# Optimization experiments

Hardware: AMD Instinct MI355X
Metric: run time of the kernel (lower is better)

## Reference

```python
import jax, jax.numpy as jnp
import numpy as np

HIDDEN = 1024
NUM_HEADS = 16
HEAD_DIM = HIDDEN // NUM_HEADS  # 64
B, S = 2, 2048


def setup_inputs() -> dict:
    key = jax.random.key(0)
    ks = jax.random.split(key, 10)
    sd = 1.0 / np.sqrt(HIDDEN)
    x = jax.random.normal(ks[0], (B, S, HIDDEN), dtype=jnp.float32)
    # per-head projections stacked over head axis: [H, hidden, head_dim]
    Wq = jax.random.normal(ks[1], (NUM_HEADS, HIDDEN, HEAD_DIM), dtype=jnp.float32) * sd
    Wk = jax.random.normal(ks[2], (NUM_HEADS, HIDDEN, HEAD_DIM), dtype=jnp.float32) * sd
    Wv = jax.random.normal(ks[3], (NUM_HEADS, HIDDEN, HEAD_DIM), dtype=jnp.float32) * sd
    bq = jax.random.normal(ks[4], (NUM_HEADS, HEAD_DIM), dtype=jnp.float32) * sd
    bk = jax.random.normal(ks[5], (NUM_HEADS, HEAD_DIM), dtype=jnp.float32) * sd
    bv = jax.random.normal(ks[6], (NUM_HEADS, HEAD_DIM), dtype=jnp.float32) * sd
    # output projection: [all_head_size, hidden]
    Wo = jax.random.normal(ks[7], (HIDDEN, HIDDEN), dtype=jnp.float32) * sd
    bo = jax.random.normal(ks[8], (HIDDEN,), dtype=jnp.float32) * sd
    return {"x": x, "Wq": Wq, "bq": bq, "Wk": Wk, "bk": bk,
            "Wv": Wv, "bv": bv, "Wo": Wo, "bo": bo}


def reference(x, Wq, bq, Wk, bk, Wv, bv, Wo, bo):
    # Fused-across-heads equivalent of the per-head Python loop.
    # q,k,v: [B, H, S, Dh]
    q = jnp.einsum('bsd,hde->bhse', x, Wq) + bq[None, :, None, :]
    k = jnp.einsum('bsd,hde->bhse', x, Wk) + bk[None, :, None, :]
    v = jnp.einsum('bsd,hde->bhse', x, Wv) + bv[None, :, None, :]
    scale = 1.0 / jnp.sqrt(jnp.asarray(HEAD_DIM, dtype=x.dtype))
    scores = jnp.einsum('bhse,bhte->bhst', q, k) * scale  # [B,H,S,S]
    probs = jax.nn.softmax(scores, axis=-1)               # dropout=0 (eval)
    ctx = jnp.einsum('bhst,bhte->bhse', probs, v)         # [B,H,S,Dh]
    # concat heads on last dim (head order matches torch.cat over heads)
    ctx = jnp.transpose(ctx, (0, 2, 1, 3)).reshape(x.shape[0], x.shape[1], -1)
    out = ctx @ Wo + bo                                   # output projection
    return out
```

## Files before the change

kernel.cpp:

```cpp
#include <hip/hip_runtime.h>
#include <cstdint>

typedef unsigned short u16;
typedef __attribute__((ext_vector_type(8))) short short8;
typedef __attribute__((ext_vector_type(4))) short short4v;
typedef __attribute__((ext_vector_type(4))) float f32x4;
typedef __attribute__((ext_vector_type(4))) unsigned short u16x4;

__device__ __forceinline__ u16 f2bf(float x) {
    unsigned int u = __float_as_uint(x);
    u += 0x7fffu + ((u >> 16) & 1u);
    return (u16)(u >> 16);
}

__device__ __forceinline__ float fexp2(float x) {
#if __has_builtin(__builtin_amdgcn_exp2f)
    return __builtin_amdgcn_exp2f(x);
#else
    return exp2f(x);
#endif
}

__device__ __forceinline__ unsigned pack_bf16(float a, float b) {
    unsigned ua = __float_as_uint(a) + 0x8000u;
    unsigned ub = __float_as_uint(b) + 0x8000u;
    return __builtin_amdgcn_perm(ub, ua, 0x07060302u);
}

#if __has_builtin(__builtin_amdgcn_mfma_f32_16x16x16bf16_1k)
__device__ __forceinline__ f32x4 mfma16(short4v a, short4v b, f32x4 c) {
    return __builtin_amdgcn_mfma_f32_16x16x16bf16_1k(a, b, c, 0, 0, 0);
}
#else
__device__ __forceinline__ f32x4 mfma16(short4v a, short4v b, f32x4 c) {
    short8 a8 = {a[0], a[1], a[2], a[3], 0, 0, 0, 0};
    short8 b8 = {b[0], b[1], b[2], b[3], 0, 0, 0, 0};
    return __builtin_amdgcn_mfma_f32_16x16x32_bf16(a8, b8, c, 0, 0, 0);
}
#endif

__device__ __forceinline__ void gload_lds16(const u16* g, u16* l) {
    __builtin_amdgcn_global_load_lds(
        (const __attribute__((address_space(1))) void*)(g),
        (__attribute__((address_space(3))) void*)(l),
        16, 0, 0);
}

__global__ __launch_bounds__(256) void prep_kernel(
    const float* __restrict__ x,
    const float* __restrict__ Wq, const float* __restrict__ Wk,
    const float* __restrict__ Wv, const float* __restrict__ Wo,
    u16* __restrict__ xb, u16* __restrict__ wqkv, u16* __restrict__ wot)
{
    __shared__ u16 tile[64][65];
    const int z = blockIdx.z;
    const int tc = threadIdx.x & 63, tr = threadIdx.x >> 6;

    if (z == 1) {
        const int blk = blockIdx.y * 16 + blockIdx.x;
        const int base = (blk * 256 + threadIdx.x) * 4;
        #pragma unroll
        for (int i = 0; i < 16; ++i) {
            const int idx = base + i * 262144;
            float4 v = *(const float4*)(x + idx);
            u16x4 o;
            o.x = f2bf(v.x); o.y = f2bf(v.y); o.z = f2bf(v.z); o.w = f2bf(v.w);
            *(u16x4*)(xb + idx) = o;
        }
        return;
    }

    const float* src;
    u16* dst;
    int C, R, rb, cb;
    if (z == 0) {
        src = Wo; dst = wot; C = 1024; R = 1024;
        rb = blockIdx.x * 64; cb = blockIdx.y * 64;
    } else {
        const float* W = (z == 2) ? Wq : (z == 3) ? Wk : Wv;
        const int head = blockIdx.y;
        src = W + head * 65536;
        dst = wqkv + (size_t)(z - 2) * 1048576 + head * 65536;
        C = 64; R = 1024;
        rb = blockIdx.x * 64; cb = 0;
    }
    #pragma unroll
    for (int i = 0; i < 64; i += 4)
        tile[tr + i][tc] = f2bf(src[(size_t)(rb + tr + i) * C + (cb + tc)]);
    __syncthreads();
    #pragma unroll
    for (int i = 0; i < 64; i += 4)
        dst[(size_t)(cb + tr + i) * R + (rb + tc)] = tile[tc][tr + i];
}

__global__ __launch_bounds__(512, 2) void gemm_qkv_kernel(
    const u16* __restrict__ X, const u16* __restrict__ W,
    const float* __restrict__ bq, const float* __restrict__ bk,
    const float* __restrict__ bv,
    u16* __restrict__ qo, u16* __restrict__ ko, u16* __restrict__ vto)
{
    __shared__ __align__(16) u16 lds[32768];
    const int tid = threadIdx.x;
    const int lane = tid & 63;
    const int wid = tid >> 6;
    const int wm = wid >> 2;
    const int wn = wid & 3;
    const int c = lane & 15, qd = lane >> 4;

    const int id = (blockIdx.x & 7) * 24 + (blockIdx.x >> 3);
    const int m0 = (id / 12) * 256;
    const int n0 = (id % 12) * 256;

    const u16* Xb = X + (size_t)m0 * 1024;
    const u16* Wb = W + (size_t)n0 * 1024;

    const int srow = tid >> 2;
    const int scg  = (lane & 3) ^ ((lane >> 3) & 3);
    const int cof = (qd ^ ((c >> 1) & 3)) * 8;
    const int rA0 = wm * 128 + c;
    const int rB0 = wn * 64 + c;

    auto stage = [&](int t, int p) {
        const int pb = p * 16384;
        #pragma unroll
        for (int j = 0; j < 2; ++j) {
            const int row = j * 128 + srow;
            const u16* gs = Xb + (size_t)row * 1024 + t * 32 + scg * 8;
            gload_lds16(gs, &lds[pb + (j * 512 + tid) * 8]);
            const u16* gw = Wb + (size_t)row * 1024 + t * 32 + scg * 8;
            gload_lds16(gw, &lds[pb + 8192 + (j * 512 + tid) * 8]);
        }
    };

    f32x4 acc[8][4];
    #pragma unroll
    for (int mi = 0; mi < 8; ++mi)
        #pragma unroll
        for (int ni = 0; ni < 4; ++ni) acc[mi][ni] = f32x4{0.f, 0.f, 0.f, 0.f};

    auto body = [&](int t) {
        const int pb = (t & 1) * 16384;
        __builtin_amdgcn_sched_barrier(0);
        __builtin_amdgcn_s_barrier();
        __builtin_amdgcn_sched_barrier(0);
        short8 af[8], bf[4];
        #pragma unroll
        for (int mi = 0; mi < 8; ++mi)
            af[mi] = *(const short8*)&lds[pb + (rA0 + mi * 16) * 32 + cof];
        #pragma unroll
        for (int ni = 0; ni < 4; ++ni)
            bf[ni] = *(const short8*)&lds[pb + 8192 + (rB0 + ni * 16) * 32 + cof];
        __builtin_amdgcn_s_setprio(1);
        #pragma unroll
        for (int mi = 0; mi < 8; ++mi)
            #pragma unroll
            for (int ni = 0; ni < 4; ++ni)
                acc[mi][ni] = __builtin_amdgcn_mfma_f32_16x16x32_bf16(af[mi], bf[ni], acc[mi][ni], 0, 0, 0);
        __builtin_amdgcn_s_setprio(0);
        __builtin_amdgcn_sched_barrier(0);
        __builtin_amdgcn_s_barrier();
    };

    stage(0, 0);
    stage(1, 1);
    __builtin_amdgcn_sched_barrier(0);

    for (int t = 0; t < 31; ++t) {
        __builtin_amdgcn_s_waitcnt(0xF74);
        body(t);
        if (t < 30) stage(t + 2, t & 1);
        __builtin_amdgcn_sched_barrier(0);
    }
    __builtin_amdgcn_s_waitcnt(0xF70);
    body(31);

    #pragma unroll
    for (int mi = 0; mi < 8; ++mi) {
        const int mbase = m0 + wm * 128 + mi * 16 + qd * 4;
        const int b = mbase >> 11;
        #pragma unroll
        for (int ni = 0; ni < 4; ++ni) {
            const int n = n0 + wn * 64 + ni * 16 + c;
            const int mat = n >> 10;
            const int idx = n & 1023;
            const int h = idx >> 6, e = idx & 63;
            const float bias = (mat == 0 ? bq : (mat == 1 ? bk : bv))[idx];
            if (mat == 2) {
                const int s = mbase & 2047;
                u16x4 pv;
                pv.x = f2bf(acc[mi][ni][0] + bias);
                pv.y = f2bf(acc[mi][ni][1] + bias);
                pv.z = f2bf(acc[mi][ni][2] + bias);
                pv.w = f2bf(acc[mi][ni][3] + bias);
                *(u16x4*)(vto + ((((size_t)(b * 16 + h) * 128 + (s >> 4)) * 64 + e) * 16
                                 + (s & 15))) = pv;
            } else {
                const float scale = (mat == 0) ? 0.18033688011112042f : 1.0f;
                u16* dst = (mat == 0) ? qo : ko;
                #pragma unroll
                for (int r = 0; r < 4; ++r) {
                    const int s = (mbase + r) & 2047;
                    dst[((size_t)((b * 16 + h) * 2048 + s)) * 64 + e] =
                        f2bf((acc[mi][ni][r] + bias) * scale);
                }
            }
        }
    }
}

__global__ __launch_bounds__(256, 3) void flash_kernel(
    const u16* __restrict__ Q,
    const u16* __restrict__ K,
    const u16* __restrict__ V2,
    u16* __restrict__ ctx)
{
    __shared__ __align__(16) char pool[34816];
    u16* stage = (u16*)pool;
    float (*Os)[64][66] = (float (*)[64][66])pool;
    float (*Ls)[64] = (float (*)[64])(pool + 33792);

    const int tid = threadIdx.x, lane = tid & 63, w = tid >> 6;
    const int c = lane & 15, qd = lane >> 4;
    const int bid = blockIdx.x;
    const int r5 = bid & 31;
    const int bh = (r5 & 7) * 4 + (r5 >> 3);
    const int q0 = (bid >> 5) * 64;
    const int b = bh >> 4, h = bh & 15;
    const u16* Qh = Q + (size_t)bh * 2048 * 64;
    const u16* Kh = K + (size_t)bh * 2048 * 64;
    const u16* Vh = V2 + (size_t)bh * 128 * 1024;

    u16* Kst = stage + w * 3072;

    const int krow8 = lane >> 3;
    const int kgc = (lane & 7) ^ (krow8 & 7);
    const int voff = c * 16 + qd * 4;

    short8 qf[4][2];
    #pragma unroll
    for (int qb = 0; qb < 4; ++qb)
        #pragma unroll
        for (int kb = 0; kb < 2; ++kb)
            qf[qb][kb] = *(const short8*)&Qh[(size_t)(q0 + qb * 16 + c) * 64 + kb * 32 + qd * 8];

    f32x4 o[4][4];
    float lsum[4];
    #pragma unroll
    for (int mt = 0; mt < 4; ++mt)
        #pragma unroll
        for (int qb = 0; qb < 4; ++qb) o[mt][qb] = f32x4{0.f, 0.f, 0.f, 0.f};
    #pragma unroll
    for (int qb = 0; qb < 4; ++qb) lsum[qb] = 0.f;

    #pragma unroll
    for (int j = 0; j < 2; ++j) {
        const int row = j * 8 + krow8;
        gload_lds16(Kh + (size_t)(w * 512 + row) * 64 + kgc * 8,
                    Kst + j * 512 + lane * 8);
    }
    short4v vA[4], vB[4];
    {
        const u16* vb = Vh + (size_t)(w * 32) * 1024 + voff;
        #pragma unroll
        for (int mt = 0; mt < 4; ++mt)
            vA[mt] = *(const short4v*)(vb + mt * 256);
    }
    #pragma unroll
    for (int j = 0; j < 2; ++j) {
        const int row = j * 8 + krow8;
        gload_lds16(Kh + (size_t)(w * 512 + 16 + row) * 64 + kgc * 8,
                    Kst + 1024 + j * 512 + lane * 8);
    }

    int cur = 0;
    auto body = [&](int it, short4v (&VC)[4], short4v (&VN)[4]) {
        u16* Kb = Kst + cur * 1024;

        __builtin_amdgcn_s_waitcnt(0xF74);
        __builtin_amdgcn_sched_barrier(0);

        short8 kf[2];
        #pragma unroll
        for (int kb = 0; kb < 2; ++kb)
            kf[kb] = *(const short8*)&Kb[c * 64 + ((4 * kb + qd) ^ (c & 7)) * 8];

        __builtin_amdgcn_sched_barrier(0);

        {
            const int itn = (it + 1) & 31;
            const u16* vb = Vh + (size_t)(w * 32 + itn) * 1024 + voff;
            #pragma unroll
            for (int mt = 0; mt < 4; ++mt)
                VN[mt] = *(const short4v*)(vb + mt * 256);
        }
        {
            const int itn = (it + 2) & 31;
            const int t0n = w * 512 + itn * 16;
            const int nslot = (cur >= 1) ? cur - 1 : 2;
            u16* Kn = Kst + nslot * 1024;
            #pragma unroll
            for (int j = 0; j < 2; ++j) {
                const int row = j * 8 + krow8;
                gload_lds16(Kh + (size_t)(t0n + row) * 64 + kgc * 8,
                            Kn + j * 512 + lane * 8);
            }
        }

        f32x4 sc[4];
        #pragma unroll
        for (int qb = 0; qb < 4; ++qb) {
            sc[qb] = f32x4{0.f, 0.f, 0.f, 0.f};
            sc[qb] = __builtin_amdgcn_mfma_f32_16x16x32_bf16(kf[0], qf[qb][0], sc[qb], 0, 0, 0);
            sc[qb] = __builtin_amdgcn_mfma_f32_16x16x32_bf16(kf[1], qf[qb][1], sc[qb], 0, 0, 0);
        }

        short4v pb[4];
        #pragma unroll
        for (int qb = 0; qb < 4; ++qb) {
            float p0 = fexp2(sc[qb][0]);
            float p1 = fexp2(sc[qb][1]);
            float p2 = fexp2(sc[qb][2]);
            float p3 = fexp2(sc[qb][3]);
            lsum[qb] += (p0 + p1) + (p2 + p3);
            unsigned d0 = pack_bf16(p0, p1);
            unsigned d1 = pack_bf16(p2, p3);
            union { unsigned u[2]; short4v s; } pu;
            pu.u[0] = d0; pu.u[1] = d1;
            pb[qb] = pu.s;
        }

        #pragma unroll
        for (int qb = 0; qb < 4; ++qb)
            #pragma unroll
            for (int mt = 0; mt < 4; ++mt)
                o[mt][qb] = mfma16(VC[mt], pb[qb], o[mt][qb]);

        cur = (cur == 2) ? 0 : cur + 1;
    };

    for (int it2 = 0; it2 < 16; ++it2) {
        body(2 * it2, vA, vB);
        body(2 * it2 + 1, vB, vA);
    }

    __builtin_amdgcn_s_waitcnt(0xF70);
    __syncthreads();

    #pragma unroll
    for (int qb = 0; qb < 4; ++qb) {
        lsum[qb] += __shfl_xor(lsum[qb], 16, 64);
        lsum[qb] += __shfl_xor(lsum[qb], 32, 64);
    }
    if (qd == 0) {
        #pragma unroll
        for (int qb = 0; qb < 4; ++qb) Ls[w][qb * 16 + c] = lsum[qb];
    }

    if (w >= 2) {
        float (*S)[66] = Os[w - 2];
        #pragma unroll
        for (int mt = 0; mt < 4; ++mt)
            #pragma unroll
            for (int qb = 0; qb < 4; ++qb)
                #pragma unroll
                for (int r = 0; r < 4; ++r)
                    S[mt * 16 + qd * 4 + r][qb * 16 + c] = o[mt][qb][r];
    }
    __syncthreads();
    if (w < 2) {
        float (*S)[66] = Os[w];
        #pragma unroll
        for (int mt = 0; mt < 4; ++mt)
            #pragma unroll
            for (int qb = 0; qb < 4; ++qb)
                #pragma unroll
                for (int r = 0; r < 4; ++r)
                    o[mt][qb][r] += S[mt * 16 + qd * 4 + r][qb * 16 + c];
    }
    __syncthreads();
    if (w == 1) {
        float (*S)[66] = Os[0];
        #pragma unroll
        for (int mt = 0; mt < 4; ++mt)
            #pragma unroll
            for (int qb = 0; qb < 4; ++qb)
                #pragma unroll
                for (int r = 0; r < 4; ++r)
                    S[mt * 16 + qd * 4 + r][qb * 16 + c] = o[mt][qb][r];
    }
    __syncthreads();
    if (w == 0) {
        float (*S)[66] = Os[0];
        float inv[4];
        #pragma unroll
        for (int qb = 0; qb < 4; ++qb) {
            int q = qb * 16 + c;
            float l = (Ls[0][q] + Ls[1][q]) + (Ls[2][q] + Ls[3][q]);
            inv[qb] = __builtin_amdgcn_rcpf(l);
        }
        #pragma unroll
        for (int mt = 0; mt < 4; ++mt)
            #pragma unroll
            for (int qb = 0; qb < 4; ++qb) {
                u16x4 ov;
                #pragma unroll
                for (int r = 0; r < 4; ++r) {
                    float v = (o[mt][qb][r] + S[mt * 16 + qd * 4 + r][qb * 16 + c]) * inv[qb];
                    ((u16*)&ov)[r] = f2bf(v);
                }
                *(u16x4*)&ctx[((size_t)(b * 2048 + q0 + qb * 16 + c)) * 1024
                              + h * 64 + mt * 16 + qd * 4] = ov;
            }
    }
}

__global__ __launch_bounds__(256, 4) void gemm_out_kernel(
    const u16* __restrict__ A, const u16* __restrict__ Wt,
    const float* __restrict__ bo, float* __restrict__ out)
{
    __shared__ __align__(16) u16 As[64 * 32];
    __shared__ __align__(16) u16 Bs[128 * 32];
    const int tid = threadIdx.x;
    const int lane = tid & 63;
    const int wv = tid >> 6;
    const int wm = wv & 1, wn = wv >> 1;
    const int m0 = blockIdx.x * 64;
    const int n0 = blockIdx.y * 128;
    const int c = lane & 15, qd = lane >> 4;

    f32x4 acc[2][4];
    #pragma unroll
    for (int a = 0; a < 2; ++a)
        #pragma unroll
        for (int b2 = 0; b2 < 4; ++b2) acc[a][b2] = f32x4{0.f, 0.f, 0.f, 0.f};

    const u16* Ab = A + (size_t)m0 * 1024;
    const u16* Wb = Wt + (size_t)n0 * 1024;

    for (int kt = 0; kt < 1024; kt += 32) {
        {
            int row = tid >> 2, part = tid & 3;
            gload_lds16(Ab + (size_t)row * 1024 + kt + part * 8, &As[tid * 8]);
        }
        #pragma unroll
        for (int i = 0; i < 2; ++i) {
            int slot = i * 256 + tid;
            int row = slot >> 2, part = slot & 3;
            gload_lds16(Wb + (size_t)row * 1024 + kt + part * 8, &Bs[slot * 8]);
        }
        __syncthreads();
        short8 af[2], bf[4];
        #pragma unroll
        for (int mt = 0; mt < 2; ++mt)
            af[mt] = *(const short8*)&As[(wm * 32 + mt * 16 + c) * 32 + qd * 8];
        #pragma unroll
        for (int nt = 0; nt < 4; ++nt)
            bf[nt] = *(const short8*)&Bs[(wn * 64 + nt * 16 + c) * 32 + qd * 8];
        #pragma unroll
        for (int mt = 0; mt < 2; ++mt)
            #pragma unroll
            for (int nt = 0; nt < 4; ++nt)
                acc[mt][nt] = __builtin_amdgcn_mfma_f32_16x16x32_bf16(af[mt], bf[nt], acc[mt][nt], 0, 0, 0);
        __syncthreads();
    }

    #pragma unroll
    for (int mt = 0; mt < 2; ++mt) {
        const int mbase = m0 + wm * 32 + mt * 16 + qd * 4;
        #pragma unroll
        for (int nt = 0; nt < 4; ++nt) {
            const int n = n0 + wn * 64 + nt * 16 + c;
            const float bias = bo[n];
            #pragma unroll
            for (int r = 0; r < 4; ++r)
                out[(size_t)(mbase + r) * 1024 + n] = acc[mt][nt][r] + bias;
        }
    }
}

extern "C" void kernel_launch(void* const* d_in, const int* in_sizes, int n_in,
                              void* d_out, int out_size, void* d_ws, size_t ws_size,
                              hipStream_t stream) {
    const float* x  = (const float*)d_in[0];
    const float* Wq = (const float*)d_in[1];
    const float* bq = (const float*)d_in[2];
    const float* Wk = (const float*)d_in[3];
    const float* bk = (const float*)d_in[4];
    const float* Wv = (const float*)d_in[5];
    const float* bv = (const float*)d_in[6];
    const float* Wo = (const float*)d_in[7];
    const float* bo = (const float*)d_in[8];
    float* out = (float*)d_out;

    u16* ws    = (u16*)d_ws;
    u16* xb    = ws;
    u16* wqkv  = xb + 4096 * 1024;
    u16* wot   = wqkv + 3072 * 1024;
    u16* qws   = wot + 1024 * 1024;
    u16* kws   = qws + 4194304;
    u16* v2ws  = kws + 4194304;
    u16* ctxws = v2ws + 4194304;

    prep_kernel<<<dim3(16, 16, 5), 256, 0, stream>>>(x, Wq, Wk, Wv, Wo, xb, wqkv, wot);
    gemm_qkv_kernel<<<192, 512, 0, stream>>>(xb, wqkv, bq, bk, bv, qws, kws, v2ws);
    flash_kernel<<<1024, 256, 0, stream>>>(qws, kws, v2ws, ctxws);
    gemm_out_kernel<<<dim3(64, 8), 256, 0, stream>>>(ctxws, wot, bo, out);
}
```

Measured before the change: 195.0 us.

## Deepen QKV GEMM K-tile to 64 and interleave staged loads with MFMA quarters

The QKV projection GEMM now stages 64-wide K tiles, twice the previous width, with a matching 8-way XOR swizzle, which doubles LDS to 128 KB. The main loop runs 16 iterations instead of 32, and each iteration is split into four MFMA quadrants. Global-to-LDS loads for the next tile are issued between quadrants, in a ping-pong schedule separated by barriers. The aim is to halve loop and barrier overhead per K and to overlap memory traffic with compute more finely. The larger LDS footprint may limit the two-blocks-per-CU occupancy the launch bounds request.

```diff
diff --git a/kernel.cpp b/kernel.cpp
--- a/kernel.cpp
+++ b/kernel.cpp
@@ -45,6 +45,10 @@
         (__attribute__((address_space(3))) void*)(l),
         16, 0, 0);
 }
+
+#define SBAR() do { __builtin_amdgcn_sched_barrier(0); \
+                    __builtin_amdgcn_s_barrier(); \
+                    __builtin_amdgcn_sched_barrier(0); } while (0)
 
 __global__ __launch_bounds__(256) void prep_kernel(
     const float* __restrict__ x,
@@ -99,7 +103,7 @@
     const float* __restrict__ bv,
     u16* __restrict__ qo, u16* __restrict__ ko, u16* __restrict__ vto)
 {
-    __shared__ __align__(16) u16 lds[32768];
+    __shared__ __align__(16) u16 lds[65536];
     const int tid = threadIdx.x;
     const int lane = tid & 63;
     const int wid = tid >> 6;
@@ -110,27 +114,26 @@
     const int id = (blockIdx.x & 7) * 24 + (blockIdx.x >> 3);
     const int m0 = (id / 12) * 256;
     const int n0 = (id % 12) * 256;
-
     const u16* Xb = X + (size_t)m0 * 1024;
     const u16* Wb = W + (size_t)n0 * 1024;
 
-    const int srow = tid >> 2;
-    const int scg  = (lane & 3) ^ ((lane >> 3) & 3);
-    const int cof = (qd ^ ((c >> 1) & 3)) * 8;
-    const int rA0 = wm * 128 + c;
-    const int rB0 = wn * 64 + c;
-
-    auto stage = [&](int t, int p) {
-        const int pb = p * 16384;
-        #pragma unroll
-        for (int j = 0; j < 2; ++j) {
-            const int row = j * 128 + srow;
-            const u16* gs = Xb + (size_t)row * 1024 + t * 32 + scg * 8;
-            gload_lds16(gs, &lds[pb + (j * 512 + tid) * 8]);
-            const u16* gw = Wb + (size_t)row * 1024 + t * 32 + scg * 8;
-            gload_lds16(gw, &lds[pb + 8192 + (j * 512 + tid) * 8]);
-        }
+    const int scg  = (tid & 7) ^ ((tid >> 3) & 7);
+    const int srow = tid >> 3;
+    const int co0 = (qd ^ (c & 7)) * 8;
+    const int co1 = ((4 + qd) ^ (c & 7)) * 8;
+    const int rA = wm * 128 + c;
+    const int rB = wn * 64 + c;
+
+    auto stageA = [&](int t, int qa) {
+        const int pb = (t & 1) * 32768;
+        gload_lds16(Xb + (size_t)(qa * 64 + srow) * 1024 + t * 64 + scg * 8,
+                    &lds[pb + (qa * 512 + tid) * 8]);
     };
+    auto stageB = [&](int t, int qb) {
+        const int pb = (t & 1) * 32768;
+        gload_lds16(Wb + (size_t)(qb * 64 + srow) * 1024 + t * 64 + scg * 8,
+                    &lds[pb + 16384 + (qb * 512 + tid) * 8]);
+    };
 
     f32x4 acc[8][4];
     #pragma unroll
@@ -138,41 +141,99 @@
         #pragma unroll
         for (int ni = 0; ni < 4; ++ni) acc[mi][ni] = f32x4{0.f, 0.f, 0.f, 0.f};
 
-    auto body = [&](int t) {
-        const int pb = (t & 1) * 16384;
-        __builtin_amdgcn_sched_barrier(0);
-        __builtin_amdgcn_s_barrier();
-        __builtin_amdgcn_sched_barrier(0);
-        short8 af[8], bf[4];
-        #pragma unroll
-        for (int mi = 0; mi < 8; ++mi)
-            af[mi] = *(const short8*)&lds[pb + (rA0 + mi * 16) * 32 + cof];
-        #pragma unroll
-        for (int ni = 0; ni < 4; ++ni)
-            bf[ni] = *(const short8*)&lds[pb + 8192 + (rB0 + ni * 16) * 32 + cof];
+    #pragma unroll
+    for (int q = 0; q < 4; ++q) stageA(0, q);
+    #pragma unroll
+    for (int q = 0; q < 4; ++q) stageB(0, q);
+    #pragma unroll
+    for (int q = 0; q < 4; ++q) stageA(1, q);
+    #pragma unroll
+    for (int q = 0; q < 4; ++q) stageB(1, q);
+    __builtin_amdgcn_s_waitcnt(0xF78);
+    SBAR();
+
+    #pragma unroll 2
+    for (int t = 0; t < 16; ++t) {
+        const int pb = (t & 1) * 32768;
+        const u16* Al = &lds[pb];
+        const u16* Bl = &lds[pb + 16384];
+
+        short8 af0[4][2], bf0[2][2];
+        #pragma unroll
+        for (int mi = 0; mi < 4; ++mi) {
+            af0[mi][0] = *(const short8*)&Al[(rA + mi * 16) * 64 + co0];
+            af0[mi][1] = *(const short8*)&Al[(rA + mi * 16) * 64 + co1];
+        }
+        #pragma unroll
+        for (int ni = 0; ni < 2; ++ni) {
+            bf0[ni][0] = *(const short8*)&Bl[(rB + ni * 16) * 64 + co0];
+            bf0[ni][1] = *(const short8*)&Bl[(rB + ni * 16) * 64 + co1];
+        }
+        SBAR();
         __builtin_amdgcn_s_setprio(1);
         #pragma unroll
-        for (int mi = 0; mi < 8; ++mi)
-            #pragma unroll
-            for (int ni = 0; ni < 4; ++ni)
-                acc[mi][ni] = __builtin_amdgcn_mfma_f32_16x16x32_bf16(af[mi], bf[ni], acc[mi][ni], 0, 0, 0);
+        for (int mi = 0; mi < 4; ++mi)
+            #pragma unroll
+            for (int ni = 0; ni < 2; ++ni) {
+                acc[mi][ni] = __builtin_amdgcn_mfma_f32_16x16x32_bf16(af0[mi][0], bf0[ni][0], acc[mi][ni], 0, 0, 0);
+                acc[mi][ni] = __builtin_amdgcn_mfma_f32_16x16x32_bf16(af0[mi][1], bf0[ni][1], acc[mi][ni], 0, 0, 0);
+            }
         __builtin_amdgcn_s_setprio(0);
-        __builtin_amdgcn_sched_barrier(0);
-        __builtin_amdgcn_s_barrier();
-    };
-
-    stage(0, 0);
-    stage(1, 1);
-    __builtin_amdgcn_sched_barrier(0);
-
-    for (int t = 0; t < 31; ++t) {
-        __builtin_amdgcn_s_waitcnt(0xF74);
-        body(t);
-        if (t < 30) stage(t + 2, t & 1);
-        __builtin_amdgcn_sched_barrier(0);
-    }
-    __builtin_amdgcn_s_waitcnt(0xF70);
-    body(31);
+        SBAR();
+
+        short8 bf1[2][2];
+        #pragma unroll
+        for (int ni = 0; ni < 2; ++ni) {
+            bf1[ni][0] = *(const short8*)&Bl[(rB + (ni + 2) * 16) * 64 + co0];
+            bf1[ni][1] = *(const short8*)&Bl[(rB + (ni + 2) * 16) * 64 + co1];
+        }
+        if (t < 14) { stageA(t + 2, 0); stageA(t + 2, 2); }
+        SBAR();
+        __builtin_amdgcn_s_setprio(1);
+        #pragma unroll
+        for (int mi = 0; mi < 4; ++mi)
+            #pragma unroll
+            for (int ni = 0; ni < 2; ++ni) {
+                acc[mi][ni + 2] = __builtin_amdgcn_mfma_f32_16x16x32_bf16(af0[mi][0], bf1[ni][0], acc[mi][ni + 2], 0, 0, 0);
+                acc[mi][ni + 2] = __builtin_amdgcn_mfma_f32_16x16x32_bf16(af0[mi][1], bf1[ni][1], acc[mi][ni + 2], 0, 0, 0);
+            }
+        __builtin_amdgcn_s_setprio(0);
+        SBAR();
+
+        short8 af1[4][2];
+        #pragma unroll
+        for (int mi = 0; mi < 4; ++mi) {
+            af1[mi][0] = *(const short8*)&Al[(rA + (mi + 4) * 16) * 64 + co0];
+            af1[mi][1] = *(const short8*)&Al[(rA + (mi + 4) * 16) * 64 + co1];
+        }
+        if (t < 14) { stageB(t + 2, 0); stageB(t + 2, 1); stageB(t + 2, 2); stageB(t + 2, 3); }
+        SBAR();
+        __builtin_amdgcn_s_setprio(1);
+        #pragma unroll
+        for (int mi = 0; mi < 4; ++mi)
+            #pragma unroll
+            for (int ni = 0; ni < 2; ++ni) {
+                acc[mi + 4][ni + 2] = __builtin_amdgcn_mfma_f32_16x16x32_bf16(af1[mi][0], bf1[ni][0], acc[mi + 4][ni + 2], 0, 0, 0);
+                acc[mi + 4][ni + 2] = __builtin_amdgcn_mfma_f32_16x16x32_bf16(af1[mi][1], bf1[ni][1], acc[mi + 4][ni + 2], 0, 0, 0);
+            }
+        __builtin_amdgcn_s_setprio(0);
+        SBAR();
+
+        if (t < 14) { stageA(t + 2, 1); stageA(t + 2, 3); }
+        SBAR();
+        __builtin_amdgcn_s_setprio(1);
+        #pragma unroll
+        for (int mi = 0; mi < 4; ++mi)
+            #pragma unroll
+            for (int ni = 0; ni < 2; ++ni) {
+                acc[mi + 4][ni] = __builtin_amdgcn_mfma_f32_16x16x32_bf16(af1[mi][0], bf0[ni][0], acc[mi + 4][ni], 0, 0, 0);
+                acc[mi + 4][ni] = __builtin_amdgcn_mfma_f32_16x16x32_bf16(af1[mi][1], bf0[ni][1], acc[mi + 4][ni], 0, 0, 0);
+            }
+        __builtin_amdgcn_s_setprio(0);
+        if (t < 14)       __builtin_amdgcn_s_waitcnt(0xF78);
+        else if (t == 14) __builtin_amdgcn_s_waitcnt(0xF70);
+        SBAR();
+    }
 
     #pragma unroll
     for (int mi = 0; mi < 8; ++mi) {
```

Result: faster. 190.7 us (-2.2%).
